# Performance work log

Hardware: AMD Instinct MI355X
Metric: run time of the kernel (lower is better)

## Reference

```python
import jax, jax.numpy as jnp
import numpy as np
from jax import lax


def conv2d(x, w, stride, pad):
    return lax.conv_general_dilated(x, w, (stride, stride), [(pad, pad), (pad, pad)],
                                    dimension_numbers=('NCHW', 'OIHW', 'NCHW'))


def maxpool3s2p1(x):
    return lax.reduce_window(x, -jnp.inf, lax.max, (1, 1, 3, 3), (1, 1, 2, 2),
                             [(0, 0), (0, 0), (1, 1), (1, 1)])


def layernorm(x, g, b):
    m = x.mean(-1, keepdims=True)
    v = x.var(-1, keepdims=True)  # torch LayerNorm uses biased variance
    return (x - m) / jnp.sqrt(v + 1e-5) * g + b


def squash(x):
    # x: [B, caps, dim]; scale each capsule by |s|^2/(1+|s|^2)/|s|
    l2 = jnp.sum(x * x, axis=2, keepdims=True)
    return x * (l2 / (1.0 + l2) / jnp.sqrt(l2))


HEADS, DIM_HEAD, INNER = 12, 64, 768


def transformer_block(x, p):
    h = layernorm(x, p['ln1_g'], p['ln1_b'])
    qkv = h @ p['qkv_w']                                   # [B,N,3*INNER]
    B, N, _ = qkv.shape
    q, k, v = [t.reshape(B, N, HEADS, DIM_HEAD).transpose(0, 2, 1, 3)
               for t in jnp.split(qkv, 3, axis=-1)]
    attn = jax.nn.softmax(jnp.einsum('bhid,bhjd->bhij', q, k) * (DIM_HEAD ** -0.5), axis=-1)
    o = jnp.einsum('bhij,bhjd->bhid', attn, v).transpose(0, 2, 1, 3).reshape(B, N, INNER)
    x = x + o @ p['out_w'] + p['out_b']
    h = layernorm(x, p['ln2_g'], p['ln2_b'])
    h = jax.nn.gelu(h @ p['ff1_w'] + p['ff1_b'], approximate=False)
    return x + h @ p['ff2_w'] + p['ff2_b']


def forward(x, conv1_w, conv2_w, pos_emb, ln1_g, ln1_b, qkv_w, out_w, out_b,
            ln2_g, ln2_b, ff1_w, ff1_b, ff2_w, ff2_b, pcaps_w, pcaps_b, caps_w, b_route):
    # ConvEmbed: conv-relu-pool x2, 40x72 -> 10x18, 64 channels
    h = jax.nn.relu(conv2d(x, conv1_w, 1, 1)); h = maxpool3s2p1(h)
    h = jax.nn.relu(conv2d(h, conv2_w, 1, 1)); h = maxpool3s2p1(h)   # [B,64,10,18]
    B = h.shape[0]
    t = h.reshape(B, 64, 180).transpose(0, 2, 1) + pos_emb           # [B,180,64]
    params = dict(ln1_g=ln1_g, ln1_b=ln1_b, qkv_w=qkv_w, out_w=out_w, out_b=out_b,
                  ln2_g=ln2_g, ln2_b=ln2_b, ff1_w=ff1_w, ff1_b=ff1_b,
                  ff2_w=ff2_w, ff2_b=ff2_b)
    step = lambda c, p: (transformer_block(c, p), None)
    for _ in range(2):  # CapsNet applies the shared 12-layer transformer twice
        t, _ = lax.scan(step, t, params)
    # reshape (B,10,18,64) -> (B,64,10,18)
    g = t.reshape(B, 10, 18, 64).transpose(0, 3, 1, 2)
    # PrimaryCaps: conv 64->256, k=3, s=2, no pad -> [B,256,4,8]
    pc = conv2d(g, pcaps_w, 2, 0) + pcaps_b[None, :, None, None]
    pc = pc.reshape(B, 32, 8, 4, 8).transpose(0, 1, 3, 4, 2).reshape(B, 1024, 8)
    caps = squash(pc)                                                # [B,1024,8]
    # CapsLayer predictions: [B,1024,3,16]
    u = jnp.einsum('bie,ieo->bio', caps, caps_w).reshape(B, 1024, 3, 16)
    # Agreement routing (3 iterations)
    c = jax.nn.softmax(b_route, axis=1)                              # [1024,3]
    v = squash(jnp.sum(c[None, :, :, None] * u, axis=1))             # [B,3,16]
    bb = jnp.broadcast_to(b_route, (B, 1024, 3))
    for _ in range(3):
        bb = bb + jnp.sum(u * v[:, None], axis=-1)
        c = jax.nn.softmax(bb, axis=-1)[..., None]
        v = squash(jnp.sum(c * u, axis=1))
    return jnp.sqrt(jnp.sum(v * v, axis=2))                          # [B,3]


def setup_inputs() -> dict:
    key = jax.random.key(0)
    ks = iter(jax.random.split(key, 24))
    nrm = lambda shape, s: jax.random.normal(next(ks), shape, jnp.float32) * s
    D, depth, MLP = 64, 12, 256
    return dict(
        x=jax.random.normal(next(ks), (256, 3, 40, 72), jnp.float32),
        conv1_w=nrm((64, 3, 3, 3), (2.0 / 27) ** 0.5),
        conv2_w=nrm((64, 64, 3, 3), (2.0 / 576) ** 0.5),
        pos_emb=nrm((1, 180, D), 0.2),
        ln1_g=jnp.ones((depth, D)), ln1_b=jnp.zeros((depth, D)),
        qkv_w=nrm((depth, D, 3 * INNER), 0.02),
        out_w=nrm((depth, INNER, D), 0.02), out_b=jnp.zeros((depth, D)),
        ln2_g=jnp.ones((depth, D)), ln2_b=jnp.zeros((depth, D)),
        ff1_w=nrm((depth, D, MLP), 0.02), ff1_b=jnp.zeros((depth, MLP)),
        ff2_w=nrm((depth, MLP, D), 0.02), ff2_b=jnp.zeros((depth, D)),
        pcaps_w=nrm((256, 64, 3, 3), (2.0 / 576) ** 0.5),
        pcaps_b=jnp.zeros((256,)),
        caps_w=jax.random.uniform(next(ks), (1024, 8, 48), jnp.float32,
                                  -(1024.0 ** -0.5), 1024.0 ** -0.5),
        b_route=jnp.zeros((1024, 3)),
    )


def reference(x, conv1_w, conv2_w, pos_emb, ln1_g, ln1_b, qkv_w, out_w, out_b,
              ln2_g, ln2_b, ff1_w, ff1_b, ff2_w, ff2_b, pcaps_w, pcaps_b, caps_w, b_route):
    return forward(x, conv1_w, conv2_w, pos_emb, ln1_g, ln1_b, qkv_w, out_w, out_b,
                   ln2_g, ln2_b, ff1_w, ff1_b, ff2_w, ff2_b, pcaps_w, pcaps_b, caps_w, b_route)
```

## Files before the change

### kernel.cpp

```cpp
#include <hip/hip_runtime.h>
#include <hip/hip_bf16.h>
#include <math.h>

#define TPB 256
typedef unsigned short u16;
typedef __attribute__((ext_vector_type(8))) short bf16x8;
typedef __attribute__((ext_vector_type(4))) float f32x4;

__device__ __forceinline__ float b2f(u16 u){ return __uint_as_float(((unsigned)u)<<16); }
__device__ __forceinline__ u16 f2b(float f){
  unsigned x = __float_as_uint(f);
  unsigned r = (x + 0x7fffu + ((x>>16)&1u)) >> 16;
  return (u16)r;
}
__device__ __forceinline__ f32x4 mfma16(bf16x8 a, bf16x8 b, f32x4 c){
  return __builtin_amdgcn_mfma_f32_16x16x32_bf16(a, b, c, 0, 0, 0);
}

__global__ __launch_bounds__(TPB) void conv1_kernel(const float* __restrict__ x,
    const float* __restrict__ w, u16* __restrict__ out){
  __shared__ float wsh[27][64];
  int tid = threadIdx.x;
  for (int idx = tid; idx < 1728; idx += TPB){
    int oc = idx / 27, i = idx - oc*27;
    wsh[i][oc] = w[idx];
  }
  __syncthreads();
  int oc = tid & 63;
  for (int it = 0; it < 32; it++){
    int pos = blockIdx.x*128 + it*4 + (tid>>6);
    int b = pos / 2880; int p = pos - b*2880;
    int oy = p / 72, ox = p - (p/72)*72;
    const float* xb = x + (size_t)b*3*2880;
    float acc = 0.f;
    #pragma unroll
    for (int dy=0; dy<3; dy++){
      int iy = oy-1+dy; if ((unsigned)iy >= 40u) continue;
      #pragma unroll
      for (int dx=0; dx<3; dx++){
        int ix = ox-1+dx; if ((unsigned)ix >= 72u) continue;
        #pragma unroll
        for (int ic=0; ic<3; ic++)
          acc += xb[ic*2880 + iy*72+ix] * wsh[(ic*3+dy)*3+dx][oc];
      }
    }
    out[(size_t)pos*64 + oc] = f2b(fmaxf(acc, 0.f));
  }
}

__global__ __launch_bounds__(TPB) void maxpool1_kernel(const u16* __restrict__ in,
    u16* __restrict__ out){
  int gid = blockIdx.x*TPB + threadIdx.x;
  int c4 = gid & 15; int p = (gid>>4) % 720; int b = gid / 11520;
  int oy = p/36, ox = p - (p/36)*36;
  ushort4 m = make_ushort4(0,0,0,0);
  #pragma unroll
  for (int dy=0; dy<3; dy++){
    int iy = oy*2-1+dy; if ((unsigned)iy >= 40u) continue;
    #pragma unroll
    for (int dx=0; dx<3; dx++){
      int ix = ox*2-1+dx; if ((unsigned)ix >= 72u) continue;
      ushort4 v = *(const ushort4*)(in + ((size_t)b*2880 + iy*72+ix)*64 + c4*4);
      m.x = v.x > m.x ? v.x : m.x;  m.y = v.y > m.y ? v.y : m.y;
      m.z = v.z > m.z ? v.z : m.z;  m.w = v.w > m.w ? v.w : m.w;
    }
  }
  *(ushort4*)(out + ((size_t)b*720 + p)*64 + c4*4) = m;
}

__global__ __launch_bounds__(TPB) void conv2_mfma(const u16* __restrict__ p1,
    const u16* __restrict__ wc2, float* __restrict__ c2){
  int s = blockIdx.y;
  int wave = threadIdx.x>>6, lane = threadIdx.x&63, q = lane>>4, li = lane&15;
  int mt = blockIdx.x*4 + wave;
  if (mt >= 45) return;
  int m0 = mt*16;
  int pos = m0 + li;
  int oy = pos/36, ox = pos - (pos/36)*36;
  const u16* ps = p1 + (size_t)s*720*64;
  f32x4 acc[4];
  #pragma unroll
  for (int nt=0;nt<4;nt++) acc[nt] = (f32x4){0.f,0.f,0.f,0.f};
  #pragma unroll
  for (int ks=0; ks<18; ks++){
    const int r9 = ks>>1;
    const int dy = r9/3, dx = r9 - 3*(r9/3);
    int k0 = ks*32 + q*8;
    int ic8 = (ks&1)*32 + q*8;
    int iy = oy-1+dy, ix = ox-1+dx;
    bf16x8 a;
    if ((unsigned)iy < 20u && (unsigned)ix < 36u)
      a = *(const bf16x8*)(ps + (size_t)(iy*36+ix)*64 + ic8);
    else
      a = (bf16x8){0,0,0,0,0,0,0,0};
    #pragma unroll
    for (int nt=0;nt<4;nt++){
      bf16x8 b = *(const bf16x8*)(wc2 + (size_t)(nt*16+li)*576 + k0);
      acc[nt] = mfma16(a, b, acc[nt]);
    }
  }
  #pragma unroll
  for (int nt=0;nt<4;nt++){
    int oc = nt*16 + li;
    #pragma unroll
    for (int r=0;r<4;r++){
      int prow = m0 + q*4 + r;
      c2[((size_t)s*720 + prow)*64 + oc] = fmaxf(acc[nt][r], 0.f);
    }
  }
}

__global__ __launch_bounds__(TPB) void pool2pos_kernel(const float* __restrict__ c2,
    const float* __restrict__ pos, float* __restrict__ t){
  int gid = blockIdx.x*TPB + threadIdx.x;
  int d4 = gid & 15; int n = (gid>>4) % 180; int b = gid / 2880;
  int oy = n/18, ox = n - (n/18)*18;
  float4 m = make_float4(0.f,0.f,0.f,0.f);
  #pragma unroll
  for (int dy=0; dy<3; dy++){
    int iy = oy*2-1+dy; if ((unsigned)iy >= 20u) continue;
    #pragma unroll
    for (int dx=0; dx<3; dx++){
      int ix = ox*2-1+dx; if ((unsigned)ix >= 36u) continue;
      float4 v = *(const float4*)(c2 + ((size_t)b*720 + iy*36+ix)*64 + d4*4);
      m.x = fmaxf(m.x, v.x); m.y = fmaxf(m.y, v.y);
      m.z = fmaxf(m.z, v.z); m.w = fmaxf(m.w, v.w);
    }
  }
  float4 pe = *(const float4*)(pos + n*64 + d4*4);
  *(float4*)(t + ((size_t)b*180 + n)*64 + d4*4) =
      make_float4(m.x+pe.x, m.y+pe.y, m.z+pe.z, m.w+pe.w);
}

__global__ __launch_bounds__(TPB) void tcvt_kernel(const float* __restrict__ src,
    u16* __restrict__ dst, int R, int C, int total){
  int gid = blockIdx.x*TPB + threadIdx.x;
  if (gid >= total) return;
  int rc = R*C;
  int l = gid / rc; int rem = gid - l*rc; int c = rem / R; int r = rem - c*R;
  dst[gid] = f2b(src[(size_t)l*rc + (size_t)r*C + c]);
}

__global__ __launch_bounds__(TPB) void tcvt_conv(const float* __restrict__ src,
    u16* __restrict__ dst, int total){
  int gid = blockIdx.x*TPB + threadIdx.x;
  if (gid >= total) return;
  int oc = gid / 576, k = gid - oc*576;
  int r9 = k >> 6, ic = k & 63;
  dst[gid] = f2b(src[oc*576 + ic*9 + r9]);
}

__global__ __launch_bounds__(TPB) void tcvt_cw(const float* __restrict__ src,
    float* __restrict__ dst){
  int gid = blockIdx.x*TPB + threadIdx.x;
  if (gid >= 393216) return;
  int i = gid / 384, rem = gid - i*384;
  int o = rem >> 3, e = rem & 7;
  dst[gid] = src[i*384 + e*48 + o];
}

__global__ __launch_bounds__(TPB) void ln_kernel(const float* __restrict__ x,
    const float* __restrict__ g, const float* __restrict__ bta, u16* __restrict__ out){
  int row = blockIdx.x*4 + (threadIdx.x>>6);
  int lane = threadIdx.x & 63;
  float v = x[(size_t)row*64 + lane];
  float s = v;
  #pragma unroll
  for (int off=32; off; off>>=1) s += __shfl_xor(s, off);
  float mean = s * (1.f/64.f);
  float d = v - mean;
  float q = d*d;
  #pragma unroll
  for (int off=32; off; off>>=1) q += __shfl_xor(q, off);
  float r = rsqrtf(q*(1.f/64.f) + 1e-5f);
  out[(size_t)row*64 + lane] = f2b(d*r*g[lane] + bta[lane]);
}

#define ATPB 384
__global__ __launch_bounds__(ATPB) void attn_fused(const u16* __restrict__ Hg,
    const u16* __restrict__ W, u16* __restrict__ Og){
  __shared__ __align__(16) u16 Kl[180][72];
  __shared__ __align__(16) u16 VT[64][200];
  __shared__ __align__(16) u16 Pw[6][16][72];
  int h = blockIdx.x, s = blockIdx.y;
  int tid = threadIdx.x, wave = tid>>6, lane = tid&63;
  int q = lane>>4, li = lane&15;
  const u16* Hb = Hg + (size_t)s*180*64;
  const u16* Wq = W + (size_t)(h*64)*64;
  const u16* Wk = W + (size_t)(768 + h*64)*64;
  const u16* Wv = W + (size_t)(1536 + h*64)*64;
  for (int p = wave; p < 12; p += 6){
    int m0 = p*16;
    int ar = m0 + li; if (ar > 179) ar = 179;
    const u16* hrow = Hb + (size_t)ar*64 + q*8;
    bf16x8 a0 = *(const bf16x8*)hrow;
    bf16x8 a1 = *(const bf16x8*)(hrow+32);
    #pragma unroll
    for (int nt=0; nt<4; nt++){
      const u16* kr = Wk + (size_t)(nt*16+li)*64 + q*8;
      bf16x8 b0 = *(const bf16x8*)kr;
      bf16x8 b1 = *(const bf16x8*)(kr+32);
      f32x4 ck = {0.f,0.f,0.f,0.f};
      ck = mfma16(a0,b0,ck); ck = mfma16(a1,b1,ck);
      #pragma unroll
      for (int r=0;r<4;r++){
        int krow = m0+q*4+r;
        if (krow < 180) Kl[krow][nt*16+li] = f2b(ck[r]);
      }
      const u16* vr = Wv + (size_t)(nt*16+li)*64 + q*8;
      bf16x8 d0 = *(const bf16x8*)vr;
      bf16x8 d1 = *(const bf16x8*)(vr+32);
      f32x4 cv = {0.f,0.f,0.f,0.f};
      cv = mfma16(a0,d0,cv); cv = mfma16(a1,d1,cv);
      #pragma unroll
      for (int r=0;r<4;r++) VT[nt*16+li][m0+q*4+r] = f2b(cv[r]);
    }
  }
  __syncthreads();
  for (int p = wave; p < 12; p += 6){
    int m0 = p*16;
    int ar = m0 + li; if (ar > 179) ar = 179;
    const u16* hrow = Hb + (size_t)ar*64 + q*8;
    bf16x8 a0 = *(const bf16x8*)hrow;
    bf16x8 a1 = *(const bf16x8*)(hrow+32);
    #pragma unroll
    for (int nt=0; nt<4; nt++){
      const u16* qr = Wq + (size_t)(nt*16+li)*64 + q*8;
      bf16x8 b0 = *(const bf16x8*)qr;
      bf16x8 b1 = *(const bf16x8*)(qr+32);
      f32x4 c = {0.f,0.f,0.f,0.f};
      c = mfma16(a0,b0,c); c = mfma16(a1,b1,c);
      #pragma unroll
      for (int r=0;r<4;r++) Pw[wave][q*4+r][nt*16+li] = f2b(c[r]*0.18033688f);
    }
    bf16x8 qf0 = *(const bf16x8*)&Pw[wave][li][q*8];
    bf16x8 qf1 = *(const bf16x8*)&Pw[wave][li][32+q*8];
    f32x4 S[12];
    #pragma unroll
    for (int t=0;t<12;t++){
      int kr0 = t*16+li; if (kr0 > 179) kr0 = 179;
      bf16x8 b0 = *(const bf16x8*)&Kl[kr0][q*8];
      bf16x8 b1 = *(const bf16x8*)&Kl[kr0][32+q*8];
      f32x4 c = {0.f,0.f,0.f,0.f};
      c = mfma16(qf0,b0,c); c = mfma16(qf1,b1,c);
      S[t] = c;
    }
    if (li >= 4){ S[11][0]=-1e30f; S[11][1]=-1e30f; S[11][2]=-1e30f; S[11][3]=-1e30f; }
    float inv[4];
    #pragma unroll
    for (int r=0;r<4;r++){
      float sum = 0.f;
      #pragma unroll
      for (int t=0;t<12;t++) sum += exp2f(S[t][r]);
      #pragma unroll
      for (int off=8; off; off>>=1) sum += __shfl_xor(sum, off);
      inv[r] = 1.f/sum;
    }
    f32x4 acc[4];
    #pragma unroll
    for (int nd=0;nd<4;nd++) acc[nd] = (f32x4){0.f,0.f,0.f,0.f};
    #pragma unroll
    for (int g=0; g<3; g++){
      #pragma unroll
      for (int t=0;t<4;t++){
        #pragma unroll
        for (int r=0;r<4;r++)
          Pw[wave][q*4+r][t*16+li] = f2b(exp2f(S[g*4+t][r]));
      }
      bf16x8 p0 = *(const bf16x8*)&Pw[wave][li][q*8];
      bf16x8 p1 = *(const bf16x8*)&Pw[wave][li][32+q*8];
      #pragma unroll
      for (int nd=0; nd<4; nd++){
        bf16x8 v0 = *(const bf16x8*)&VT[nd*16+li][g*64 + q*8];
        bf16x8 v1 = *(const bf16x8*)&VT[nd*16+li][g*64 + 32 + q*8];
        acc[nd] = mfma16(p0, v0, acc[nd]);
        acc[nd] = mfma16(p1, v1, acc[nd]);
      }
    }
    #pragma unroll
    for (int nd=0; nd<4; nd++){
      #pragma unroll
      for (int r=0;r<4;r++)
        Pw[wave][q*4+r][nd*16+li] = f2b(acc[nd][r]*inv[r]);
    }
    int g8 = lane>>3, u8 = lane&7;
    #pragma unroll
    for (int it2=0; it2<2; it2++){
      int rr = it2*8 + g8;
      int row = m0 + rr;
      bf16x8 ov = *(const bf16x8*)&Pw[wave][rr][u8*8];
      if (row < 180)
        *(bf16x8*)(Og + (size_t)(s*180+row)*768 + h*64 + u8*8) = ov;
    }
  }
}

__global__ __launch_bounds__(TPB) void gemm_outp(const u16* __restrict__ Og,
    const u16* __restrict__ WOT, const float* __restrict__ outb,
    const float* __restrict__ lng, const float* __restrict__ lnb,
    float* __restrict__ t, u16* __restrict__ HgOut){
  int wave = threadIdx.x>>6, lane = threadIdx.x&63, q = lane>>4, li = lane&15;
  int m0 = blockIdx.x*64 + wave*16;
  f32x4 acc[4];
  #pragma unroll
  for (int nd=0;nd<4;nd++) acc[nd] = (f32x4){0.f,0.f,0.f,0.f};
  for (int kb=0; kb<24; kb++){
    bf16x8 a = *(const bf16x8*)(Og + (size_t)(m0+li)*768 + kb*32 + q*8);
    #pragma unroll
    for (int nd=0;nd<4;nd++){
      bf16x8 b = *(const bf16x8*)(WOT + (size_t)(nd*16+li)*768 + kb*32 + q*8);
      acc[nd] = mfma16(a, b, acc[nd]);
    }
  }
  float tv[4][4]; float gv[4], bvn[4];
  #pragma unroll
  for (int nd=0;nd<4;nd++){
    int col = nd*16 + li;
    float bv = outb[col];
    gv[nd] = lng[col]; bvn[nd] = lnb[col];
    #pragma unroll
    for (int r=0;r<4;r++){
      size_t off = (size_t)(m0 + q*4 + r)*64 + col;
      float v = t[off] + acc[nd][r] + bv;
      t[off] = v;
      tv[nd][r] = v;
    }
  }
  #pragma unroll
  for (int r=0;r<4;r++){
    float s = tv[0][r]+tv[1][r]+tv[2][r]+tv[3][r];
    #pragma unroll
    for (int off=8; off; off>>=1) s += __shfl_xor(s, off);
    float mean = s*(1.f/64.f);
    float qs = 0.f;
    #pragma unroll
    for (int nd=0;nd<4;nd++){ float d = tv[nd][r]-mean; qs += d*d; }
    #pragma unroll
    for (int off=8; off; off>>=1) qs += __shfl_xor(qs, off);
    float rinv = rsqrtf(qs*(1.f/64.f) + 1e-5f);
    size_t rowoff = (size_t)(m0 + q*4 + r)*64;
    #pragma unroll
    for (int nd=0;nd<4;nd++){
      int col = nd*16 + li;
      HgOut[rowoff + col] = f2b((tv[nd][r]-mean)*rinv*gv[nd] + bvn[nd]);
    }
  }
}

__global__ __launch_bounds__(TPB) void gemm_ffn(const u16* __restrict__ Hg,
    const u16* __restrict__ W1, const float* __restrict__ b1,
    const u16* __restrict__ W2, const float* __restrict__ b2,
    const float* __restrict__ lng, const float* __restrict__ lnb,
    float* __restrict__ t, u16* __restrict__ HgOut){
  __shared__ __align__(16) u16 panel[4][16][264];
  int wave = threadIdx.x>>6, lane = threadIdx.x&63, q = lane>>4, li = lane&15;
  int m0 = blockIdx.x*64 + wave*16;
  const u16* arow = Hg + (size_t)(m0+li)*64 + q*8;
  bf16x8 a0 = *(const bf16x8*)arow;
  bf16x8 a1 = *(const bf16x8*)(arow + 32);
  for (int nt=0; nt<16; nt++){
    const u16* brow = W1 + (size_t)(nt*16+li)*64 + q*8;
    bf16x8 b0 = *(const bf16x8*)brow;
    bf16x8 b1v = *(const bf16x8*)(brow + 32);
    f32x4 c = {0.f,0.f,0.f,0.f};
    c = mfma16(a0, b0, c);
    c = mfma16(a1, b1v, c);
    int col = nt*16 + li;
    float bv = b1[col];
    #pragma unroll
    for (int r=0;r<4;r++){
      float v = c[r] + bv;
      v = v*0.5f*(1.f + erff(v*0.70710678118f));
      panel[wave][q*4+r][col] = f2b(v);
    }
  }
  bf16x8 ap[8];
  #pragma unroll
  for (int kb=0;kb<8;kb++) ap[kb] = *(const bf16x8*)&panel[wave][li][kb*32 + q*8];
  f32x4 acc[4];
  #pragma unroll
  for (int nd=0;nd<4;nd++) acc[nd] = (f32x4){0.f,0.f,0.f,0.f};
  #pragma unroll
  for (int kb=0; kb<8; kb++){
    #pragma unroll
    for (int nd=0;nd<4;nd++){
      bf16x8 b = *(const bf16x8*)(W2 + (size_t)(nd*16+li)*256 + kb*32 + q*8);
      acc[nd] = mfma16(ap[kb], b, acc[nd]);
    }
  }
  float tv[4][4]; float gv[4], bvn[4];
  #pragma unroll
  for (int nd=0;nd<4;nd++){
    int col = nd*16 + li;
    float bv = b2[col];
    gv[nd] = lng[col]; bvn[nd] = lnb[col];
    #pragma unroll
    for (int r=0;r<4;r++){
      size_t off = (size_t)(m0 + q*4 + r)*64 + col;
      float v = t[off] + acc[nd][r] + bv;
      t[off] = v;
      tv[nd][r] = v;
    }
  }
  #pragma unroll
  for (int r=0;r<4;r++){
    float s = tv[0][r]+tv[1][r]+tv[2][r]+tv[3][r];
    #pragma unroll
    for (int off=8; off; off>>=1) s += __shfl_xor(s, off);
    float mean = s*(1.f/64.f);
    float qs = 0.f;
    #pragma unroll
    for (int nd=0;nd<4;nd++){ float d = tv[nd][r]-mean; qs += d*d; }
    #pragma unroll
    for (int off=8; off; off>>=1) qs += __shfl_xor(qs, off);
    float rinv = rsqrtf(qs*(1.f/64.f) + 1e-5f);
    size_t rowoff = (size_t)(m0 + q*4 + r)*64;
    #pragma unroll
    for (int nd=0;nd<4;nd++){
      int col = nd*16 + li;
      HgOut[rowoff + col] = f2b((tv[nd][r]-mean)*rinv*gv[nd] + bvn[nd]);
    }
  }
}

__global__ __launch_bounds__(TPB) void pcaps_mfma(const float* __restrict__ t,
    const u16* __restrict__ wpc, const float* __restrict__ bias, float* __restrict__ caps){
  int b = blockIdx.x;
  int wave = threadIdx.x>>6, lane = threadIdx.x&63, q = lane>>4, li = lane&15;
  int mt = wave & 1, nh = wave >> 1;
  const float* tb = t + (size_t)b*180*64;
  int pos_a = mt*16 + li;
  int oy_a = pos_a >> 3, ox_a = pos_a & 7;
  f32x4 acc[8];
  #pragma unroll
  for (int nt=0;nt<8;nt++) acc[nt] = (f32x4){0.f,0.f,0.f,0.f};
  for (int ks=0; ks<18; ks++){
    int k0 = ks*32 + q*8;
    int r9 = k0 >> 6, ic = k0 & 63;
    int dy = r9/3, dx = r9 - 3*dy;
    const float* src = tb + ((2*oy_a+dy)*18 + (2*ox_a+dx))*64 + ic;
    float4 f0 = *(const float4*)src;
    float4 f1 = *(const float4*)(src+4);
    bf16x8 a;
    a[0]=(short)f2b(f0.x); a[1]=(short)f2b(f0.y); a[2]=(short)f2b(f0.z); a[3]=(short)f2b(f0.w);
    a[4]=(short)f2b(f1.x); a[5]=(short)f2b(f1.y); a[6]=(short)f2b(f1.z); a[7]=(short)f2b(f1.w);
    #pragma unroll
    for (int nt=0;nt<8;nt++){
      bf16x8 bb8 = *(const bf16x8*)(wpc + (size_t)(nh*128 + nt*16 + li)*576 + k0);
      acc[nt] = mfma16(a, bb8, acc[nt]);
    }
  }
  #pragma unroll
  for (int nt=0;nt<8;nt++){
    int oc = nh*128 + nt*16 + li;
    float bv = bias[oc];
    #pragma unroll
    for (int r=0;r<4;r++){
      int prow = mt*16 + q*4 + r;
      float val = acc[nt][r] + bv;
      float l2 = val*val;
      l2 += __shfl_xor(l2, 1);
      l2 += __shfl_xor(l2, 2);
      l2 += __shfl_xor(l2, 4);
      float sc = (l2 > 0.f) ? l2/((1.f+l2)*sqrtf(l2)) : 0.f;
      caps[((size_t)b*1024 + (oc>>3)*32 + prow)*8 + (oc&7)] = val*sc;
    }
  }
}

__global__ __launch_bounds__(TPB) void u_kernel(const float* __restrict__ caps,
    const float* __restrict__ cwT, float* __restrict__ u){
  int gid = blockIdx.x*TPB + threadIdx.x;
  int o = gid % 48; int i = (gid/48) & 1023; int b = gid/(48*1024);
  const float* cp = caps + ((size_t)b*1024 + i)*8;
  const float* wp = cwT + ((size_t)i*48 + o)*8;
  float4 c0 = *(const float4*)cp, c1 = *(const float4*)(cp+4);
  float4 w0 = *(const float4*)wp, w1 = *(const float4*)(wp+4);
  u[gid] = c0.x*w0.x + c0.y*w0.y + c0.z*w0.z + c0.w*w0.w
         + c1.x*w1.x + c1.y*w1.y + c1.z*w1.z + c1.w*w1.w;
}

__global__ __launch_bounds__(TPB) void routing_kernel(const float* __restrict__ u,
    const float* __restrict__ b_route, float* __restrict__ out){
  __shared__ float bb[3072];
  __shared__ float vsh[48];
  __shared__ float red[4][48];
  __shared__ float ssh[48];
  int b = blockIdx.x, tid = threadIdx.x;
  const float* ub = u + (size_t)b*49152;
  for (int idx=tid; idx<3072; idx+=TPB) bb[idx] = b_route[idx];
  __syncthreads();
  for (int it=0; it<4; it++){
    if (it > 0){
      for (int idx=tid; idx<3072; idx+=TPB){
        int i = idx/3, j = idx - i*3;
        const float* up = ub + i*48 + j*16;
        float s = 0.f;
        #pragma unroll
        for (int e=0;e<16;e++) s += up[e]*vsh[j*16+e];
        bb[idx] += s;
      }
      __syncthreads();
    }
    float acc[48];
    #pragma unroll
    for (int q2=0;q2<48;q2++) acc[q2] = 0.f;
    for (int i=tid; i<1024; i+=TPB){
      float b0=bb[i*3], b1=bb[i*3+1], b2v=bb[i*3+2];
      float m = fmaxf(b0, fmaxf(b1, b2v));
      float e0=__expf(b0-m), e1=__expf(b1-m), e2=__expf(b2v-m);
      float inv = 1.f/(e0+e1+e2);
      float c0=e0*inv, c1=e1*inv, c2=e2*inv;
      const float* up = ub + i*48;
      #pragma unroll
      for (int e=0;e<16;e++){
        acc[e]    += c0*up[e];
        acc[16+e] += c1*up[16+e];
        acc[32+e] += c2*up[32+e];
      }
    }
    #pragma unroll
    for (int q2=0;q2<48;q2++){
      float v = acc[q2];
      #pragma unroll
      for (int off=32; off; off>>=1) v += __shfl_xor(v, off);
      if ((tid&63)==0) red[tid>>6][q2] = v;
    }
    __syncthreads();
    if (tid < 48) ssh[tid] = red[0][tid]+red[1][tid]+red[2][tid]+red[3][tid];
    __syncthreads();
    if (tid < 48){
      int j = tid >> 4;
      float l2 = 0.f;
      #pragma unroll
      for (int e=0;e<16;e++) l2 += ssh[j*16+e]*ssh[j*16+e];
      float sc = (l2 > 0.f) ? l2/((1.f+l2)*sqrtf(l2)) : 0.f;
      vsh[tid] = ssh[tid]*sc;
    }
    __syncthreads();
  }
  if (tid < 3){
    float l2 = 0.f;
    #pragma unroll
    for (int e=0;e<16;e++) l2 += vsh[tid*16+e]*vsh[tid*16+e];
    out[b*3+tid] = sqrtf(l2);
  }
}

extern "C" void kernel_launch(void* const* d_in, const int* in_sizes, int n_in,
                              void* d_out, int out_size, void* d_ws, size_t ws_size,
                              hipStream_t stream){
  const float* x       = (const float*)d_in[0];
  const float* conv1_w = (const float*)d_in[1];
  const float* conv2_w = (const float*)d_in[2];
  const float* pos_emb = (const float*)d_in[3];
  const float* ln1_g   = (const float*)d_in[4];
  const float* ln1_b   = (const float*)d_in[5];
  const float* qkv_w   = (const float*)d_in[6];
  const float* out_w   = (const float*)d_in[7];
  const float* out_b   = (const float*)d_in[8];
  const float* ln2_g   = (const float*)d_in[9];
  const float* ln2_b   = (const float*)d_in[10];
  const float* ff1_w   = (const float*)d_in[11];
  const float* ff1_b   = (const float*)d_in[12];
  const float* ff2_w   = (const float*)d_in[13];
  const float* ff2_b   = (const float*)d_in[14];
  const float* pc_w    = (const float*)d_in[15];
  const float* pc_b    = (const float*)d_in[16];
  const float* caps_w  = (const float*)d_in[17];
  const float* b_route = (const float*)d_in[18];
  float* out = (float*)d_out;

  char* ws = (char*)d_ws;
  float* t_buf = (float*)(ws);
  u16*  Hg    = (u16*)(ws + 11796480);
  u16*  WQKVT = (u16*)(ws + 17694720);
  u16*  WOT   = (u16*)(ws + 21233664);
  u16*  WF1T  = (u16*)(ws + 22413312);
  u16*  WF2T  = (u16*)(ws + 22806528);
  u16*  wpc   = (u16*)(ws + 23199744);
  float* cwT  = (float*)(ws + 23494656);
  u16*  wc2   = (u16*)(ws + 25067520);
  char* win   = ws + 25141248;
  u16*  Og    = (u16*)win;
  u16*  p1out = (u16*)win;
  u16*  c1out = (u16*)(win + 23592960);
  float* c2out = (float*)(win + 23592960);
  float* caps  = (float*)(win);
  float* u_buf = (float*)(win + 8388608);

  tcvt_kernel<<<6912, TPB, 0, stream>>>(qkv_w, WQKVT, 64, 2304, 12*64*2304);
  tcvt_kernel<<<2304, TPB, 0, stream>>>(out_w, WOT, 768, 64, 12*768*64);
  tcvt_kernel<<<768, TPB, 0, stream>>>(ff1_w, WF1T, 64, 256, 12*64*256);
  tcvt_kernel<<<768, TPB, 0, stream>>>(ff2_w, WF2T, 256, 64, 12*256*64);
  tcvt_conv<<<576, TPB, 0, stream>>>(pc_w, wpc, 147456);
  tcvt_conv<<<144, TPB, 0, stream>>>(conv2_w, wc2, 36864);
  tcvt_cw<<<1536, TPB, 0, stream>>>(caps_w, cwT);

  for (int c = 0; c < 4; c++){
    conv1_kernel<<<1440, TPB, 0, stream>>>(x + (size_t)c*64*3*2880, conv1_w, c1out);
    maxpool1_kernel<<<2880, TPB, 0, stream>>>(c1out, p1out + (size_t)c*64*720*64);
  }
  conv2_mfma<<<dim3(12,256), TPB, 0, stream>>>(p1out, wc2, c2out);
  pool2pos_kernel<<<2880, TPB, 0, stream>>>(c2out, pos_emb, t_buf);

  ln_kernel<<<11520, TPB, 0, stream>>>(t_buf, ln1_g, ln1_b, Hg);
  for (int itr=0; itr<24; itr++){
    int l = itr % 12;
    int ln = (itr+1) % 12;
    attn_fused<<<dim3(12,256), ATPB, 0, stream>>>(Hg, WQKVT + (size_t)l*2304*64, Og);
    gemm_outp<<<720, TPB, 0, stream>>>(Og, WOT + (size_t)l*64*768, out_b + l*64,
                                       ln2_g + l*64, ln2_b + l*64, t_buf, Hg);
    gemm_ffn<<<720, TPB, 0, stream>>>(Hg, WF1T + (size_t)l*256*64, ff1_b + l*256,
                                      WF2T + (size_t)l*64*256, ff2_b + l*64,
                                      ln1_g + ln*64, ln1_b + ln*64, t_buf, Hg);
  }

  pcaps_mfma<<<256, TPB, 0, stream>>>(t_buf, wpc, pc_b, caps);
  u_kernel<<<49152, TPB, 0, stream>>>(caps, cwT, u_buf);
  routing_kernel<<<256, TPB, 0, stream>>>(u_buf, b_route, out);
}
```

Before: 6.111 ms.

## Fuse out-projection and FFN into one kernel; shrink attention blocks to four waves

```diff
diff --git a/kernel.cpp b/kernel.cpp
--- a/kernel.cpp
+++ b/kernel.cpp
@@ -176,12 +176,11 @@
   out[(size_t)row*64 + lane] = f2b(d*r*g[lane] + bta[lane]);
 }
 
-#define ATPB 384
-__global__ __launch_bounds__(ATPB) void attn_fused(const u16* __restrict__ Hg,
+__global__ __launch_bounds__(TPB) void attn_fused(const u16* __restrict__ Hg,
     const u16* __restrict__ W, u16* __restrict__ Og){
   __shared__ __align__(16) u16 Kl[180][72];
   __shared__ __align__(16) u16 VT[64][200];
-  __shared__ __align__(16) u16 Pw[6][16][72];
+  __shared__ __align__(16) u16 Pw[4][16][72];
   int h = blockIdx.x, s = blockIdx.y;
   int tid = threadIdx.x, wave = tid>>6, lane = tid&63;
   int q = lane>>4, li = lane&15;
@@ -189,7 +188,7 @@
   const u16* Wq = W + (size_t)(h*64)*64;
   const u16* Wk = W + (size_t)(768 + h*64)*64;
   const u16* Wv = W + (size_t)(1536 + h*64)*64;
-  for (int p = wave; p < 12; p += 6){
+  for (int p = wave; p < 12; p += 4){
     int m0 = p*16;
     int ar = m0 + li; if (ar > 179) ar = 179;
     const u16* hrow = Hb + (size_t)ar*64 + q*8;
@@ -217,7 +216,7 @@
     }
   }
   __syncthreads();
-  for (int p = wave; p < 12; p += 6){
+  for (int p = wave; p < 12; p += 4){
     int m0 = p*16;
     int ar = m0 + li; if (ar > 179) ar = 179;
     const u16* hrow = Hb + (size_t)ar*64 + q*8;
@@ -295,69 +294,62 @@
   }
 }
 
-__global__ __launch_bounds__(TPB) void gemm_outp(const u16* __restrict__ Og,
+__global__ __launch_bounds__(TPB) void gemm_outp_ffn(const u16* __restrict__ Og,
     const u16* __restrict__ WOT, const float* __restrict__ outb,
-    const float* __restrict__ lng, const float* __restrict__ lnb,
-    float* __restrict__ t, u16* __restrict__ HgOut){
-  int wave = threadIdx.x>>6, lane = threadIdx.x&63, q = lane>>4, li = lane&15;
-  int m0 = blockIdx.x*64 + wave*16;
-  f32x4 acc[4];
-  #pragma unroll
-  for (int nd=0;nd<4;nd++) acc[nd] = (f32x4){0.f,0.f,0.f,0.f};
-  for (int kb=0; kb<24; kb++){
-    bf16x8 a = *(const bf16x8*)(Og + (size_t)(m0+li)*768 + kb*32 + q*8);
-    #pragma unroll
-    for (int nd=0;nd<4;nd++){
-      bf16x8 b = *(const bf16x8*)(WOT + (size_t)(nd*16+li)*768 + kb*32 + q*8);
-      acc[nd] = mfma16(a, b, acc[nd]);
-    }
-  }
-  float tv[4][4]; float gv[4], bvn[4];
-  #pragma unroll
-  for (int nd=0;nd<4;nd++){
-    int col = nd*16 + li;
-    float bv = outb[col];
-    gv[nd] = lng[col]; bvn[nd] = lnb[col];
-    #pragma unroll
-    for (int r=0;r<4;r++){
-      size_t off = (size_t)(m0 + q*4 + r)*64 + col;
-      float v = t[off] + acc[nd][r] + bv;
-      t[off] = v;
-      tv[nd][r] = v;
-    }
-  }
-  #pragma unroll
-  for (int r=0;r<4;r++){
-    float s = tv[0][r]+tv[1][r]+tv[2][r]+tv[3][r];
-    #pragma unroll
-    for (int off=8; off; off>>=1) s += __shfl_xor(s, off);
-    float mean = s*(1.f/64.f);
-    float qs = 0.f;
-    #pragma unroll
-    for (int nd=0;nd<4;nd++){ float d = tv[nd][r]-mean; qs += d*d; }
-    #pragma unroll
-    for (int off=8; off; off>>=1) qs += __shfl_xor(qs, off);
-    float rinv = rsqrtf(qs*(1.f/64.f) + 1e-5f);
-    size_t rowoff = (size_t)(m0 + q*4 + r)*64;
-    #pragma unroll
-    for (int nd=0;nd<4;nd++){
-      int col = nd*16 + li;
-      HgOut[rowoff + col] = f2b((tv[nd][r]-mean)*rinv*gv[nd] + bvn[nd]);
-    }
-  }
-}
-
-__global__ __launch_bounds__(TPB) void gemm_ffn(const u16* __restrict__ Hg,
+    const float* __restrict__ ln2g, const float* __restrict__ ln2b,
     const u16* __restrict__ W1, const float* __restrict__ b1,
     const u16* __restrict__ W2, const float* __restrict__ b2,
-    const float* __restrict__ lng, const float* __restrict__ lnb,
+    const float* __restrict__ ln1g, const float* __restrict__ ln1b,
     float* __restrict__ t, u16* __restrict__ HgOut){
   __shared__ __align__(16) u16 panel[4][16][264];
   int wave = threadIdx.x>>6, lane = threadIdx.x&63, q = lane>>4, li = lane&15;
   int m0 = blockIdx.x*64 + wave*16;
-  const u16* arow = Hg + (size_t)(m0+li)*64 + q*8;
-  bf16x8 a0 = *(const bf16x8*)arow;
-  bf16x8 a1 = *(const bf16x8*)(arow + 32);
+  f32x4 acc[4];
+  #pragma unroll
+  for (int nd=0;nd<4;nd++) acc[nd] = (f32x4){0.f,0.f,0.f,0.f};
+  for (int kb=0; kb<24; kb++){
+    bf16x8 a = *(const bf16x8*)(Og + (size_t)(m0+li)*768 + kb*32 + q*8);
+    #pragma unroll
+    for (int nd=0;nd<4;nd++){
+      bf16x8 b = *(const bf16x8*)(WOT + (size_t)(nd*16+li)*768 + kb*32 + q*8);
+      acc[nd] = mfma16(a, b, acc[nd]);
+    }
+  }
+  {
+    float tv[4][4];
+    #pragma unroll
+    for (int nd=0;nd<4;nd++){
+      int col = nd*16 + li;
+      float bv = outb[col];
+      #pragma unroll
+      for (int r=0;r<4;r++){
+        size_t off = (size_t)(m0 + q*4 + r)*64 + col;
+        float v = t[off] + acc[nd][r] + bv;
+        t[off] = v;
+        tv[nd][r] = v;
+      }
+    }
+    #pragma unroll
+    for (int r=0;r<4;r++){
+      float s = tv[0][r]+tv[1][r]+tv[2][r]+tv[3][r];
+      #pragma unroll
+      for (int off=8; off; off>>=1) s += __shfl_xor(s, off);
+      float mean = s*(1.f/64.f);
+      float qs = 0.f;
+      #pragma unroll
+      for (int nd=0;nd<4;nd++){ float d = tv[nd][r]-mean; qs += d*d; }
+      #pragma unroll
+      for (int off=8; off; off>>=1) qs += __shfl_xor(qs, off);
+      float rinv = rsqrtf(qs*(1.f/64.f) + 1e-5f);
+      #pragma unroll
+      for (int nd=0;nd<4;nd++){
+        int col = nd*16 + li;
+        panel[wave][q*4+r][col] = f2b((tv[nd][r]-mean)*rinv*ln2g[col] + ln2b[col]);
+      }
+    }
+  }
+  bf16x8 a0 = *(const bf16x8*)&panel[wave][li][q*8];
+  bf16x8 a1 = *(const bf16x8*)&panel[wave][li][32 + q*8];
   for (int nt=0; nt<16; nt++){
     const u16* brow = W1 + (size_t)(nt*16+li)*64 + q*8;
     bf16x8 b0 = *(const bf16x8*)brow;
@@ -377,7 +369,6 @@
   bf16x8 ap[8];
   #pragma unroll
   for (int kb=0;kb<8;kb++) ap[kb] = *(const bf16x8*)&panel[wave][li][kb*32 + q*8];
-  f32x4 acc[4];
   #pragma unroll
   for (int nd=0;nd<4;nd++) acc[nd] = (f32x4){0.f,0.f,0.f,0.f};
   #pragma unroll
@@ -393,7 +384,7 @@
   for (int nd=0;nd<4;nd++){
     int col = nd*16 + li;
     float bv = b2[col];
-    gv[nd] = lng[col]; bvn[nd] = lnb[col];
+    gv[nd] = ln1g[col]; bvn[nd] = ln1b[col];
     #pragma unroll
     for (int r=0;r<4;r++){
       size_t off = (size_t)(m0 + q*4 + r)*64 + col;
@@ -608,12 +599,12 @@
   for (int itr=0; itr<24; itr++){
     int l = itr % 12;
     int ln = (itr+1) % 12;
-    attn_fused<<<dim3(12,256), ATPB, 0, stream>>>(Hg, WQKVT + (size_t)l*2304*64, Og);
-    gemm_outp<<<720, TPB, 0, stream>>>(Og, WOT + (size_t)l*64*768, out_b + l*64,
-                                       ln2_g + l*64, ln2_b + l*64, t_buf, Hg);
-    gemm_ffn<<<720, TPB, 0, stream>>>(Hg, WF1T + (size_t)l*256*64, ff1_b + l*256,
-                                      WF2T + (size_t)l*64*256, ff2_b + l*64,
-                                      ln1_g + ln*64, ln1_b + ln*64, t_buf, Hg);
+    attn_fused<<<dim3(12,256), TPB, 0, stream>>>(Hg, WQKVT + (size_t)l*2304*64, Og);
+    gemm_outp_ffn<<<720, TPB, 0, stream>>>(Og, WOT + (size_t)l*64*768, out_b + l*64,
+                                           ln2_g + l*64, ln2_b + l*64,
+                                           WF1T + (size_t)l*256*64, ff1_b + l*256,
+                                           WF2T + (size_t)l*64*256, ff2_b + l*64,
+                                           ln1_g + ln*64, ln1_b + ln*64, t_buf, Hg);
   }
 
   pcaps_mfma<<<256, TPB, 0, stream>>>(t_buf, wpc, pc_b, caps);
```

New measurement: 5.234 ms. -14.4%, faster.
